# Performance work log

Measured on AMD Instinct MI355X. Metric: run time of the kernel, lower is better.

## Reference

```python
import jax, jax.numpy as jnp
import numpy as np

B, N = 64, 1024

def setup_inputs() -> dict:
    key = jax.random.key(0)
    ks = jax.random.split(key, 8)
    x = jax.random.normal(ks[0], (B, N, 3), dtype=jnp.float32)
    adj = jax.random.uniform(ks[1], (B, N, N), dtype=jnp.float32)
    # Linear params stored as [in, out]; torch Linear init scale ~1/sqrt(in)
    W1 = jax.random.normal(ks[2], (3, 10), dtype=jnp.float32) / np.sqrt(3.0)
    b1 = jax.random.normal(ks[3], (10,), dtype=jnp.float32) * 0.1
    W2 = jax.random.normal(ks[4], (10, 10), dtype=jnp.float32) / np.sqrt(10.0)
    b2 = jax.random.normal(ks[5], (10,), dtype=jnp.float32) * 0.1
    W3 = jax.random.normal(ks[6], (10, 2), dtype=jnp.float32) / np.sqrt(10.0)
    b3 = jax.random.normal(ks[7], (2,), dtype=jnp.float32) * 0.1
    return {"x": x, "adj": adj, "W1": W1, "b1": b1, "W2": W2, "b2": b2, "W3": W3, "b3": b3}

def reference(x, adj, W1, b1, W2, b2, W3, b3):
    # round 1: message MLP then dense aggregation
    m1 = jnp.tanh(x @ W1 + b1)              # [B, N, 10]
    h = jnp.einsum('bnm,bmd->bnd', adj, m1) # [B, N, 10]
    # round 2
    m2 = jnp.tanh(h @ W2 + b2)              # [B, N, 10]
    h = jnp.einsum('bnm,bmd->bnd', adj, m2) # [B, N, 10]
    # sum pooling over nodes + readout
    pooled = h.sum(axis=1)                  # [B, 10]
    return pooled @ W3 + b3                 # [B, 2]
```

## Files before the change

### kernel.cpp

```cpp
#include <hip/hip_runtime.h>


typedef __attribute__((ext_vector_type(8))) short short8;
typedef __attribute__((ext_vector_type(4))) float f32x4;

__device__ __forceinline__ unsigned short f2bf(float f) {
    unsigned int u = __float_as_uint(f);
    u += 0x7FFFu + ((u >> 16) & 1u);
    return (unsigned short)(u >> 16);
}

__global__ __launch_bounds__(256) void k_mlp1(const float* __restrict__ x,
                                              const float* __restrict__ W1,
                                              const float* __restrict__ b1,
                                              unsigned short* __restrict__ bpack) {
    int g = blockIdx.x * 256 + threadIdx.x;
    int slot = g & 63;
    int b_kc = g >> 6;
    int d = slot & 15, q = slot >> 4;
    int kc = b_kc & 31, b = b_kc >> 5;
    int m0 = kc * 32 + q * 8;
    const float* xp = x + (size_t)(b * 1024 + m0) * 3;
    float w0 = 0.f, w1 = 0.f, w2 = 0.f, bb = 0.f;
    if (d < 10) { w0 = W1[d]; w1 = W1[10 + d]; w2 = W1[20 + d]; bb = b1[d]; }
    unsigned int o[8];
#pragma unroll
    for (int j = 0; j < 8; ++j) {
        float v = 0.f;
        if (d < 10) v = tanhf(xp[j*3] * w0 + xp[j*3+1] * w1 + xp[j*3+2] * w2 + bb);
        o[j] = f2bf(v);
    }
    uint4 pk;
    pk.x = o[0] | (o[1] << 16);
    pk.y = o[2] | (o[3] << 16);
    pk.z = o[4] | (o[5] << 16);
    pk.w = o[6] | (o[7] << 16);
    *(uint4*)(bpack + (size_t)g * 8) = pk;
}

__global__ __launch_bounds__(256) void k_agg(const float* __restrict__ adj,
                                             const unsigned short* __restrict__ bpack,
                                             float* __restrict__ h_ws,
                                             float* __restrict__ cs_part) {
    __shared__ __align__(16) unsigned short aT[64 * 128];
    __shared__ __align__(16) unsigned short bP[16384];
    __shared__ float csb[4 * 128];

    const int t = threadIdx.x;
    const int b = blockIdx.x >> 4;
    const int tile = blockIdx.x & 15;
    const int n0 = tile * 64;
    const int l = t & 63, w = t >> 6;
    const int rgrp = t >> 5;
    const int c32 = t & 31;

    {
        const uint4* bg = (const uint4*)(bpack + (size_t)b * 16384);
        uint4* bl = (uint4*)bP;
#pragma unroll
        for (int i = 0; i < 8; ++i) bl[i * 256 + t] = bg[i * 256 + t];
    }

    f32x4 acc = {0.f, 0.f, 0.f, 0.f};

    for (int kstep = 0; kstep < 8; ++kstep) {
        float cs0 = 0.f, cs1 = 0.f, cs2 = 0.f, cs3 = 0.f;
#pragma unroll
        for (int i = 0; i < 8; ++i) {
            int row = i * 8 + rgrp;
            int col = c32 * 4;
            const float4 a = *(const float4*)(adj
                + (size_t)(b * 1024 + n0 + row) * 1024 + kstep * 128 + col);
            cs0 += a.x; cs1 += a.y; cs2 += a.z; cs3 += a.w;
            unsigned int lo = f2bf(a.x) | ((unsigned)f2bf(a.y) << 16);
            unsigned int hi = f2bf(a.z) | ((unsigned)f2bf(a.w) << 16);
            unsigned bo = (unsigned)(row * 256 + col * 2);
            bo ^= (unsigned)((row & 7) << 4);
            *(uint2*)((char*)aT + bo) = make_uint2(lo, hi);
        }
        cs0 += __shfl_xor(cs0, 32); cs1 += __shfl_xor(cs1, 32);
        cs2 += __shfl_xor(cs2, 32); cs3 += __shfl_xor(cs3, 32);
        if (l < 32)
            *(float4*)&csb[w * 128 + l * 4] = make_float4(cs0, cs1, cs2, cs3);
        __syncthreads();
#pragma unroll
        for (int kc = 0; kc < 4; ++kc) {
            int lrow = w * 16 + (l & 15);
            unsigned bo = (unsigned)(lrow * 256 + kc * 64 + (l >> 4) * 16);
            bo ^= (unsigned)((lrow & 7) << 4);
            short8 af = *(const short8*)((char*)aT + bo);
            short8 bf = *((const short8*)bP + (kstep * 4 + kc) * 64 + l);
            acc = __builtin_amdgcn_mfma_f32_16x16x32_bf16(af, bf, acc, 0, 0, 0);
        }
        if (t < 128) {
            float s = csb[t] + csb[128 + t] + csb[256 + t] + csb[384 + t];
            cs_part[(((size_t)b * 16 + tile) * 8 + kstep) * 128 + t] = s;
        }
        __syncthreads();
    }
    {
        int col = l & 15, rb = (l >> 4) * 4;
#pragma unroll
        for (int r = 0; r < 4; ++r) {
            int n = n0 + w * 16 + rb + r;
            h_ws[((size_t)(b * 1024 + n) << 4) + col] = acc[r];
        }
    }
}

__global__ __launch_bounds__(256) void k_read(const float* __restrict__ h_ws,
                                              const float* __restrict__ cs_part,
                                              const float* __restrict__ W2,
                                              const float* __restrict__ b2,
                                              const float* __restrict__ W3,
                                              const float* __restrict__ b3,
                                              float* __restrict__ out) {
    int b = blockIdx.x, t = threadIdx.x;
    float pool[10];
#pragma unroll
    for (int d = 0; d < 10; ++d) pool[d] = 0.f;

    for (int it = 0; it < 4; ++it) {
        int m = it * 256 + t;
        float cs = 0.f;
#pragma unroll
        for (int tile = 0; tile < 16; ++tile)
            cs += cs_part[(((size_t)b * 16 + tile) * 8 + (m >> 7)) * 128 + (m & 127)];
        const float* hp = h_ws + ((size_t)(b * 1024 + m) << 4);
        float hv[10];
#pragma unroll
        for (int d = 0; d < 10; ++d) hv[d] = hp[d];
#pragma unroll
        for (int dp = 0; dp < 10; ++dp) {
            float s = b2[dp];
#pragma unroll
            for (int d = 0; d < 10; ++d) s += hv[d] * W2[d * 10 + dp];
            pool[dp] += cs * tanhf(s);
        }
    }
#pragma unroll
    for (int d = 0; d < 10; ++d) {
        float v = pool[d];
        v += __shfl_xor(v, 1);  v += __shfl_xor(v, 2);  v += __shfl_xor(v, 4);
        v += __shfl_xor(v, 8);  v += __shfl_xor(v, 16); v += __shfl_xor(v, 32);
        pool[d] = v;
    }
    __shared__ float red[4][10];
    int l = t & 63, w = t >> 6;
    if (l == 0) {
#pragma unroll
        for (int d = 0; d < 10; ++d) red[w][d] = pool[d];
    }
    __syncthreads();
    if (t < 2) {
        float s = b3[t];
#pragma unroll
        for (int dp = 0; dp < 10; ++dp) {
            float p = red[0][dp] + red[1][dp] + red[2][dp] + red[3][dp];
            s += p * W3[dp * 2 + t];
        }
        out[b * 2 + t] = s;
    }
}

extern "C" void kernel_launch(void* const* d_in, const int* in_sizes, int n_in,
                              void* d_out, int out_size, void* d_ws, size_t ws_size,
                              hipStream_t stream) {
    (void)in_sizes; (void)n_in; (void)out_size; (void)ws_size;
    const float* x   = (const float*)d_in[0];
    const float* adj = (const float*)d_in[1];
    const float* W1  = (const float*)d_in[2];
    const float* b1  = (const float*)d_in[3];
    const float* W2  = (const float*)d_in[4];
    const float* b2  = (const float*)d_in[5];
    const float* W3  = (const float*)d_in[6];
    const float* b3  = (const float*)d_in[7];
    float* out = (float*)d_out;

    char* ws = (char*)d_ws;
    unsigned short* bpack = (unsigned short*)ws;
    float* h_ws    = (float*)(ws + (2u << 20));
    float* cs_part = (float*)(ws + (6u << 20));

    k_mlp1<<<512, 256, 0, stream>>>(x, W1, b1, bpack);
    k_agg<<<1024, 256, 0, stream>>>(adj, bpack, h_ws, cs_part);
    k_read<<<64, 256, 0, stream>>>(h_ws, cs_part, W2, b2, W3, b3, out);
}
```

Baseline: 389.8 us.

## Double-buffer adj tiles in LDS and read B fragments directly from global

The aggregation kernel now prefetches the next 64x128 adjacency slice into registers while running MFMAs on the current slice, using two LDS buffers so only one barrier per k-step is needed. The 32KB LDS staging of the packed message matrix is removed, and B fragments are loaded straight from global (L2-resident) memory. The aim is to hide HBM latency behind compute and conversion and to reduce LDS footprint for occupancy. The cost is higher register pressure from eight in-flight float4 loads, plus global-latency B loads inside the MFMA loop.

```diff
diff --git a/kernel.cpp b/kernel.cpp
--- a/kernel.cpp
+++ b/kernel.cpp
@@ -38,13 +38,32 @@
     *(uint4*)(bpack + (size_t)g * 8) = pk;
 }
 
+__device__ __forceinline__ void cvt_store(const float4* a, unsigned short* aTb,
+                                          float* csbb, int rgrp, int c32,
+                                          int w, int l) {
+    float cs0 = 0.f, cs1 = 0.f, cs2 = 0.f, cs3 = 0.f;
+#pragma unroll
+    for (int i = 0; i < 8; ++i) {
+        int row = i * 8 + rgrp;
+        cs0 += a[i].x; cs1 += a[i].y; cs2 += a[i].z; cs3 += a[i].w;
+        unsigned int lo = f2bf(a[i].x) | ((unsigned)f2bf(a[i].y) << 16);
+        unsigned int hi = f2bf(a[i].z) | ((unsigned)f2bf(a[i].w) << 16);
+        unsigned bo = (unsigned)(row * 256 + c32 * 8);
+        bo ^= (unsigned)((row & 7) << 4);
+        *(uint2*)((char*)aTb + bo) = make_uint2(lo, hi);
+    }
+    cs0 += __shfl_xor(cs0, 32); cs1 += __shfl_xor(cs1, 32);
+    cs2 += __shfl_xor(cs2, 32); cs3 += __shfl_xor(cs3, 32);
+    if (l < 32)
+        *(float4*)&csbb[w * 128 + l * 4] = make_float4(cs0, cs1, cs2, cs3);
+}
+
 __global__ __launch_bounds__(256) void k_agg(const float* __restrict__ adj,
                                              const unsigned short* __restrict__ bpack,
                                              float* __restrict__ h_ws,
                                              float* __restrict__ cs_part) {
-    __shared__ __align__(16) unsigned short aT[64 * 128];
-    __shared__ __align__(16) unsigned short bP[16384];
-    __shared__ float csb[4 * 128];
+    __shared__ __align__(16) unsigned short aT[2][64 * 128];
+    __shared__ float csb[2][4 * 128];
 
     const int t = threadIdx.x;
     const int b = blockIdx.x >> 4;
@@ -54,49 +73,48 @@
     const int rgrp = t >> 5;
     const int c32 = t & 31;
 
+    const float* adj_base = adj + (size_t)(b * 1024 + n0) * 1024;
+    const short8* bfrag = (const short8*)(bpack + (size_t)b * 16384);
+
     {
-        const uint4* bg = (const uint4*)(bpack + (size_t)b * 16384);
-        uint4* bl = (uint4*)bP;
-#pragma unroll
-        for (int i = 0; i < 8; ++i) bl[i * 256 + t] = bg[i * 256 + t];
-    }
+        float4 a0[8];
+#pragma unroll
+        for (int i = 0; i < 8; ++i)
+            a0[i] = *(const float4*)(adj_base + (size_t)(i * 8 + rgrp) * 1024 + c32 * 4);
+        cvt_store(a0, aT[0], csb[0], rgrp, c32, w, l);
+    }
+    __syncthreads();
 
     f32x4 acc = {0.f, 0.f, 0.f, 0.f};
-
-    for (int kstep = 0; kstep < 8; ++kstep) {
-        float cs0 = 0.f, cs1 = 0.f, cs2 = 0.f, cs3 = 0.f;
-#pragma unroll
-        for (int i = 0; i < 8; ++i) {
-            int row = i * 8 + rgrp;
-            int col = c32 * 4;
-            const float4 a = *(const float4*)(adj
-                + (size_t)(b * 1024 + n0 + row) * 1024 + kstep * 128 + col);
-            cs0 += a.x; cs1 += a.y; cs2 += a.z; cs3 += a.w;
-            unsigned int lo = f2bf(a.x) | ((unsigned)f2bf(a.y) << 16);
-            unsigned int hi = f2bf(a.z) | ((unsigned)f2bf(a.w) << 16);
-            unsigned bo = (unsigned)(row * 256 + col * 2);
-            bo ^= (unsigned)((row & 7) << 4);
-            *(uint2*)((char*)aT + bo) = make_uint2(lo, hi);
-        }
-        cs0 += __shfl_xor(cs0, 32); cs1 += __shfl_xor(cs1, 32);
-        cs2 += __shfl_xor(cs2, 32); cs3 += __shfl_xor(cs3, 32);
-        if (l < 32)
-            *(float4*)&csb[w * 128 + l * 4] = make_float4(cs0, cs1, cs2, cs3);
-        __syncthreads();
+    int p = 0;
+    const int lrow = w * 16 + (l & 15);
+    const int lcol0 = (l >> 4) * 16;
+
+    for (int k = 0; k < 8; ++k) {
+        float4 nx[8];
+        if (k < 7) {
+#pragma unroll
+            for (int i = 0; i < 8; ++i)
+                nx[i] = *(const float4*)(adj_base
+                    + (size_t)(i * 8 + rgrp) * 1024 + (k + 1) * 128 + c32 * 4);
+        }
 #pragma unroll
         for (int kc = 0; kc < 4; ++kc) {
-            int lrow = w * 16 + (l & 15);
-            unsigned bo = (unsigned)(lrow * 256 + kc * 64 + (l >> 4) * 16);
+            unsigned bo = (unsigned)(lrow * 256 + kc * 64 + lcol0);
             bo ^= (unsigned)((lrow & 7) << 4);
-            short8 af = *(const short8*)((char*)aT + bo);
-            short8 bf = *((const short8*)bP + (kstep * 4 + kc) * 64 + l);
+            short8 af = *(const short8*)((char*)aT[p] + bo);
+            short8 bf = bfrag[(k * 4 + kc) * 64 + l];
             acc = __builtin_amdgcn_mfma_f32_16x16x32_bf16(af, bf, acc, 0, 0, 0);
         }
         if (t < 128) {
-            float s = csb[t] + csb[128 + t] + csb[256 + t] + csb[384 + t];
-            cs_part[(((size_t)b * 16 + tile) * 8 + kstep) * 128 + t] = s;
-        }
-        __syncthreads();
+            float s = csb[p][t] + csb[p][128 + t] + csb[p][256 + t] + csb[p][384 + t];
+            cs_part[(((size_t)b * 16 + tile) * 8 + k) * 128 + t] = s;
+        }
+        if (k < 7) {
+            cvt_store(nx, aT[p ^ 1], csb[p ^ 1], rgrp, c32, w, l);
+            __syncthreads();
+            p ^= 1;
+        }
     }
     {
         int col = l & 15, rb = (l >> 4) * 4;
```

After: 383.3 us. About the same (-1.7%).
